# Kernel tuning notes

Measured on AMD Instinct MI355X. Metric: run time of the kernel, lower is better.

The kernel has to match this reference:

```python
import jax, jax.numpy as jnp
import numpy as np


def setup_inputs() -> dict:
    key = jax.random.key(0)
    x = jax.random.normal(key, (1024, 65536), dtype=jnp.float32)
    return {"input": x}


def reference(input) -> jnp.ndarray:
    B = input.shape[0]
    flat = input.reshape(B, -1)            # [B, N]
    N = flat.shape[1]
    idx = int(N * 0.8)                      # 80th-percentile position (ascending sort)
    cutoff = jnp.sort(flat, axis=-1)[:, idx]  # [B]
    cutoff = jax.lax.stop_gradient(cutoff)
    # broadcast cutoff back over all non-batch dims
    cutoff = cutoff.reshape((B,) + (1,) * (input.ndim - 1))
    return jax.nn.relu(input - cutoff)
```

## Files before the change

### kernel.cpp

```cpp
#include <hip/hip_runtime.h>


#define TPB1  1024
#define NB    4096
#define CAP   8192
#define TINY  64
#define BLO   0.72f
#define BHI   0.98f

#define TPB2  256
#define VPT   16

__device__ __forceinline__ unsigned f2ord(float f) {
    unsigned u = __float_as_uint(f);
    return (u & 0x80000000u) ? ~u : (u | 0x80000000u);
}
__device__ __forceinline__ float ord2f(unsigned u) {
    unsigned b = (u & 0x80000000u) ? (u ^ 0x80000000u) : ~u;
    return __uint_as_float(b);
}

__global__ __launch_bounds__(TPB1)
void cutoff_kernel(const float* __restrict__ in, float* __restrict__ cut,
                   int N, int k) {
    const int row  = blockIdx.x;
    const int tid  = threadIdx.x;
    const int lane = tid & 63;
    const int nv   = N >> 2;
    const float SCALE = (float)NB / (BHI - BLO);
    const float4* __restrict__ rowv = (const float4*)(in + (size_t)row * (size_t)N);

    __shared__ unsigned hist[NB];
    __shared__ unsigned cand[CAP];
    __shared__ unsigned part[TPB1];
    __shared__ unsigned tiny[TINY];
    __shared__ unsigned s_cnt, s_below, s_cum, s_tc;
    __shared__ int s_bin, s_fb;
    __shared__ float s_cut;

    for (int i = tid; i < NB; i += TPB1) hist[i] = 0u;
    if (tid == 0) { s_cnt = 0u; s_below = 0u; s_tc = 0u; s_fb = 0; }
    __syncthreads();

    unsigned below = 0;
    for (int i = tid; i < nv; i += TPB1) {
        float4 v = rowv[i];
        float vals[4] = {v.x, v.y, v.z, v.w};
        #pragma unroll
        for (int j = 0; j < 4; ++j) {
            float f = vals[j];
            below += (f < BLO) ? 1u : 0u;
            bool pred = (f >= BLO) && (f < BHI);
            unsigned long long m = __ballot(pred);
            if (m) {
                int leader = __ffsll((long long)m) - 1;
                unsigned base = 0;
                if (lane == leader) base = atomicAdd(&s_cnt, (unsigned)__popcll(m));
                base = __shfl(base, leader);
                if (pred) {
                    unsigned p = base + (unsigned)__popcll(m & ((1ull << lane) - 1ull));
                    if (p < CAP) cand[p] = __float_as_uint(f) | 0x80000000u;
                    int b = (int)((f - BLO) * SCALE);
                    b = b < 0 ? 0 : (b >= NB ? NB - 1 : b);
                    atomicAdd(&hist[b], 1u);
                }
            }
        }
    }
    #pragma unroll
    for (int o = 32; o > 0; o >>= 1) below += __shfl_down(below, o);
    if (lane == 0) atomicAdd(&s_below, below);
    __syncthreads();

    const unsigned M0 = s_cnt;
    const long long r2ll = (long long)k - (long long)s_below;

    if (M0 > CAP || r2ll < 0 || r2ll >= (long long)M0) {
        if (tid == 0) s_fb = 1;
    } else {
        const unsigned r2 = (unsigned)r2ll;
        const int base4 = tid * 4;
        unsigned s = hist[base4] + hist[base4 + 1] + hist[base4 + 2] + hist[base4 + 3];
        part[tid] = s;
        __syncthreads();
        for (int off = 1; off < TPB1; off <<= 1) {
            unsigned add = (tid >= off) ? part[tid - off] : 0u;
            __syncthreads();
            part[tid] += add;
            __syncthreads();
        }
        unsigned incl = part[tid], excl = incl - s;
        if (r2 >= excl && r2 < incl) {
            unsigned c = excl;
            #pragma unroll
            for (int j = 0; j < 4; ++j) {
                unsigned h = hist[base4 + j];
                if (r2 < c + h) { s_bin = base4 + j; s_cum = c; break; }
                c += h;
            }
        }
        __syncthreads();
        const int bin = s_bin;
        const unsigned r3 = r2 - s_cum;
        if (tid < 64) {
            for (unsigned i = (unsigned)lane; i < M0; i += 64u) {
                unsigned u = cand[i];
                float f = __uint_as_float(u ^ 0x80000000u);
                int b = (int)((f - BLO) * SCALE);
                b = b < 0 ? 0 : (b >= NB ? NB - 1 : b);
                bool pred = (b == bin);
                unsigned long long mm = __ballot(pred);
                if (mm) {
                    int leader = __ffsll((long long)mm) - 1;
                    unsigned tb = 0;
                    if (lane == leader) tb = atomicAdd(&s_tc, (unsigned)__popcll(mm));
                    tb = __shfl(tb, leader);
                    if (pred) {
                        unsigned p = tb + (unsigned)__popcll(mm & ((1ull << lane) - 1ull));
                        if (p < TINY) tiny[p] = u;
                    }
                }
            }
            unsigned c = s_tc;
            if (c > TINY) { if (lane == 0) s_fb = 1; }
            else {
                unsigned uj = (lane < (int)c) ? tiny[lane] : 0xFFFFFFFFu;
                unsigned less = 0, eq = 0;
                for (unsigned i2 = 0; i2 < c; ++i2) {
                    unsigned ui = tiny[i2];
                    less += (ui < uj) ? 1u : 0u;
                    eq   += (ui == uj) ? 1u : 0u;
                }
                bool cond = (lane < (int)c) && (less <= r3) && (r3 < less + eq);
                unsigned long long cm = __ballot(cond);
                if (cond && lane == __ffsll((long long)cm) - 1)
                    s_cut = __uint_as_float(uj ^ 0x80000000u);
            }
        }
    }
    __syncthreads();

    if (s_fb) {
        for (int i = tid; i < NB; i += TPB1) hist[i] = 0u;
        if (tid == 0) s_cnt = 0u;
        __syncthreads();
        for (int i = tid; i < nv; i += TPB1) {
            float4 v = rowv[i];
            float vals[4] = {v.x, v.y, v.z, v.w};
            #pragma unroll
            for (int j = 0; j < 4; ++j) atomicAdd(&hist[f2ord(vals[j]) >> 20], 1u);
        }
        __syncthreads();
        const int base4 = tid * 4;
        unsigned s = hist[base4] + hist[base4 + 1] + hist[base4 + 2] + hist[base4 + 3];
        part[tid] = s;
        __syncthreads();
        for (int off = 1; off < TPB1; off <<= 1) {
            unsigned add = (tid >= off) ? part[tid - off] : 0u;
            __syncthreads();
            part[tid] += add;
            __syncthreads();
        }
        const unsigned rk = (unsigned)k;
        unsigned incl = part[tid], excl = incl - s;
        if (rk >= excl && rk < incl) {
            unsigned c = excl;
            #pragma unroll
            for (int j = 0; j < 4; ++j) {
                unsigned h = hist[base4 + j];
                if (rk < c + h) { s_bin = base4 + j; s_cum = c; break; }
                c += h;
            }
        }
        __syncthreads();
        const unsigned bin = (unsigned)s_bin;
        for (int i = tid; i < nv; i += TPB1) {
            float4 v = rowv[i];
            float vals[4] = {v.x, v.y, v.z, v.w};
            #pragma unroll
            for (int j = 0; j < 4; ++j) {
                unsigned u = f2ord(vals[j]);
                bool pred = ((u >> 20) == bin);
                unsigned long long m = __ballot(pred);
                if (m) {
                    int leader = __ffsll((long long)m) - 1;
                    unsigned b2 = 0;
                    if (lane == leader) b2 = atomicAdd(&s_cnt, (unsigned)__popcll(m));
                    b2 = __shfl(b2, leader);
                    if (pred) {
                        unsigned p = b2 + (unsigned)__popcll(m & ((1ull << lane) - 1ull));
                        if (p < CAP) cand[p] = u;
                    }
                }
            }
        }
        __syncthreads();
        if (tid < 64) {
            unsigned M2 = s_cnt; if (M2 > CAP) M2 = CAP;
            unsigned prefix = bin;
            unsigned rr = (unsigned)k - s_cum;
            for (int bit = 19; bit >= 0; --bit) {
                unsigned want0 = prefix << 1;
                unsigned cnt = 0;
                for (unsigned i = (unsigned)lane; i < M2; i += 64u)
                    if ((cand[i] >> bit) == want0) cnt++;
                #pragma unroll
                for (int o = 32; o > 0; o >>= 1) cnt += __shfl_down(cnt, o);
                cnt = __shfl(cnt, 0);
                if (rr < cnt) prefix = want0;
                else { rr -= cnt; prefix = want0 | 1u; }
            }
            if (lane == 0) s_cut = ord2f(prefix);
        }
        __syncthreads();
    }

    if (tid == 0) cut[row] = s_cut;
}

__global__ __launch_bounds__(TPB2)
void relu_kernel(const float* __restrict__ in, const float* __restrict__ cut,
                 float* __restrict__ out, int N) {
    const int f4PerBlock = TPB2 * VPT;
    const int bpr = (N >> 2) / f4PerBlock;
    const int row = blockIdx.x / bpr;
    const float c = cut[row];
    const size_t base = (size_t)blockIdx.x * (size_t)f4PerBlock + threadIdx.x;
    const float4* __restrict__ iv = (const float4*)in;
    float4* __restrict__ ov = (float4*)out;
    #pragma unroll
    for (int j = 0; j < VPT; ++j) {
        size_t idx = base + (size_t)j * TPB2;
        float4 v = iv[idx];
        float4 o;
        o.x = fmaxf(v.x - c, 0.0f);
        o.y = fmaxf(v.y - c, 0.0f);
        o.z = fmaxf(v.z - c, 0.0f);
        o.w = fmaxf(v.w - c, 0.0f);
        ov[idx] = o;
    }
}

extern "C" void kernel_launch(void* const* d_in, const int* in_sizes, int n_in,
                              void* d_out, int out_size, void* d_ws, size_t ws_size,
                              hipStream_t stream) {
    const float* in = (const float*)d_in[0];
    float* out = (float*)d_out;
    float* cut = (float*)d_ws;
    const int N = 65536;
    const int B = in_sizes[0] / N;
    const int k = (int)(((long long)N * 4) / 5);

    cutoff_kernel<<<dim3(B), dim3(TPB1), 0, stream>>>(in, cut, N, k);

    const int totalF4 = (B * N) >> 2;
    const int blocks2 = totalF4 / (TPB2 * VPT);
    relu_kernel<<<dim3(blocks2), dim3(TPB2), 0, stream>>>(in, cut, out, N);
}
```

Baseline: 500.8 us.

## Shrink cutoff blocks, defer histogram to candidates, use wave-shuffle scan selection

```diff
diff --git a/kernel.cpp b/kernel.cpp
--- a/kernel.cpp
+++ b/kernel.cpp
@@ -1,9 +1,9 @@
 #include <hip/hip_runtime.h>
 
 
-#define TPB1  1024
-#define NB    4096
-#define CAP   8192
+#define TPB1  512
+#define NB    2048
+#define CAP   6144
 #define TINY  64
 #define BLO   0.72f
 #define BHI   0.98f
@@ -20,7 +20,39 @@
     return __uint_as_float(b);
 }
 
-__global__ __launch_bounds__(TPB1)
+__device__ __forceinline__ void hist_select(const unsigned* hist, unsigned r, int tid,
+                                            unsigned* wsum, unsigned* wbase,
+                                            int* s_bin, unsigned* s_cum) {
+    const int lane = tid & 63, wid = tid >> 6;
+    const int b0 = tid * (NB / TPB1);
+    unsigned h0 = hist[b0], h1 = hist[b0+1], h2 = hist[b0+2], h3 = hist[b0+3];
+    unsigned s = h0 + h1 + h2 + h3;
+    unsigned incl = s;
+    #pragma unroll
+    for (int off = 1; off < 64; off <<= 1) {
+        unsigned t = __shfl_up(incl, off);
+        if (lane >= off) incl += t;
+    }
+    if (lane == 63) wsum[wid] = incl;
+    __syncthreads();
+    if (tid == 0) {
+        unsigned c = 0;
+        #pragma unroll
+        for (int w = 0; w < TPB1/64; ++w) { wbase[w] = c; c += wsum[w]; }
+    }
+    __syncthreads();
+    unsigned excl = wbase[wid] + incl - s;
+    if (r >= excl && r < excl + s) {
+        unsigned c = excl;
+        if (r < c + h0)        { *s_bin = b0;     *s_cum = c; }
+        else { c += h0; if (r < c + h1) { *s_bin = b0 + 1; *s_cum = c; }
+        else { c += h1; if (r < c + h2) { *s_bin = b0 + 2; *s_cum = c; }
+        else { c += h2;                   *s_bin = b0 + 3; *s_cum = c; } } }
+    }
+    __syncthreads();
+}
+
+__global__ __launch_bounds__(TPB1, 8)
 void cutoff_kernel(const float* __restrict__ in, float* __restrict__ cut,
                    int N, int k) {
     const int row  = blockIdx.x;
@@ -32,8 +64,8 @@
 
     __shared__ unsigned hist[NB];
     __shared__ unsigned cand[CAP];
-    __shared__ unsigned part[TPB1];
     __shared__ unsigned tiny[TINY];
+    __shared__ unsigned wsum[TPB1/64], wbase[TPB1/64];
     __shared__ unsigned s_cnt, s_below, s_cum, s_tc;
     __shared__ int s_bin, s_fb;
     __shared__ float s_cut;
@@ -50,20 +82,9 @@
         for (int j = 0; j < 4; ++j) {
             float f = vals[j];
             below += (f < BLO) ? 1u : 0u;
-            bool pred = (f >= BLO) && (f < BHI);
-            unsigned long long m = __ballot(pred);
-            if (m) {
-                int leader = __ffsll((long long)m) - 1;
-                unsigned base = 0;
-                if (lane == leader) base = atomicAdd(&s_cnt, (unsigned)__popcll(m));
-                base = __shfl(base, leader);
-                if (pred) {
-                    unsigned p = base + (unsigned)__popcll(m & ((1ull << lane) - 1ull));
-                    if (p < CAP) cand[p] = __float_as_uint(f) | 0x80000000u;
-                    int b = (int)((f - BLO) * SCALE);
-                    b = b < 0 ? 0 : (b >= NB ? NB - 1 : b);
-                    atomicAdd(&hist[b], 1u);
-                }
+            if (f >= BLO && f < BHI) {
+                unsigned p = atomicAdd(&s_cnt, 1u);
+                if (p < CAP) cand[p] = __float_as_uint(f);
             }
         }
     }
@@ -74,144 +95,75 @@
 
     const unsigned M0 = s_cnt;
     const long long r2ll = (long long)k - (long long)s_below;
-
-    if (M0 > CAP || r2ll < 0 || r2ll >= (long long)M0) {
-        if (tid == 0) s_fb = 1;
-    } else {
+    const bool fast = (M0 <= CAP) && (r2ll >= 0) && (r2ll < (long long)M0);
+
+    if (fast) {
         const unsigned r2 = (unsigned)r2ll;
-        const int base4 = tid * 4;
-        unsigned s = hist[base4] + hist[base4 + 1] + hist[base4 + 2] + hist[base4 + 3];
-        part[tid] = s;
+        for (unsigned i = tid; i < M0; i += TPB1) {
+            float f = __uint_as_float(cand[i]);
+            int b = (int)((f - BLO) * SCALE);
+            b = b < 0 ? 0 : (b >= NB ? NB - 1 : b);
+            atomicAdd(&hist[b], 1u);
+        }
         __syncthreads();
-        for (int off = 1; off < TPB1; off <<= 1) {
-            unsigned add = (tid >= off) ? part[tid - off] : 0u;
-            __syncthreads();
-            part[tid] += add;
-            __syncthreads();
-        }
-        unsigned incl = part[tid], excl = incl - s;
-        if (r2 >= excl && r2 < incl) {
-            unsigned c = excl;
-            #pragma unroll
-            for (int j = 0; j < 4; ++j) {
-                unsigned h = hist[base4 + j];
-                if (r2 < c + h) { s_bin = base4 + j; s_cum = c; break; }
-                c += h;
-            }
-        }
-        __syncthreads();
+        hist_select(hist, r2, tid, wsum, wbase, &s_bin, &s_cum);
         const int bin = s_bin;
         const unsigned r3 = r2 - s_cum;
-        if (tid < 64) {
-            for (unsigned i = (unsigned)lane; i < M0; i += 64u) {
-                unsigned u = cand[i];
-                float f = __uint_as_float(u ^ 0x80000000u);
-                int b = (int)((f - BLO) * SCALE);
-                b = b < 0 ? 0 : (b >= NB ? NB - 1 : b);
-                bool pred = (b == bin);
-                unsigned long long mm = __ballot(pred);
-                if (mm) {
-                    int leader = __ffsll((long long)mm) - 1;
-                    unsigned tb = 0;
-                    if (lane == leader) tb = atomicAdd(&s_tc, (unsigned)__popcll(mm));
-                    tb = __shfl(tb, leader);
-                    if (pred) {
-                        unsigned p = tb + (unsigned)__popcll(mm & ((1ull << lane) - 1ull));
-                        if (p < TINY) tiny[p] = u;
-                    }
+        for (unsigned i = tid; i < M0; i += TPB1) {
+            unsigned u = cand[i];
+            float f = __uint_as_float(u);
+            int b = (int)((f - BLO) * SCALE);
+            b = b < 0 ? 0 : (b >= NB ? NB - 1 : b);
+            if (b == bin) { unsigned p = atomicAdd(&s_tc, 1u); if (p < TINY) tiny[p] = u; }
+        }
+        __syncthreads();
+        const unsigned c = s_tc;
+        if (c > TINY) { if (tid == 0) s_fb = 1; }
+        else if (tid < 64) {
+            unsigned uj = (lane < (int)c) ? tiny[lane] : 0xFFFFFFFFu;
+            unsigned less = 0, eq = 0;
+            for (unsigned i2 = 0; i2 < c; ++i2) {
+                unsigned ui = tiny[i2];
+                less += (ui < uj) ? 1u : 0u;
+                eq   += (ui == uj) ? 1u : 0u;
+            }
+            bool cond = (lane < (int)c) && (less <= r3) && (r3 < less + eq);
+            unsigned long long cm = __ballot(cond);
+            if (cond && lane == __ffsll((long long)cm) - 1)
+                s_cut = __uint_as_float(uj);
+        }
+    } else {
+        if (tid == 0) s_fb = 1;
+    }
+    __syncthreads();
+
+    if (s_fb) {
+        unsigned prefix = 0;
+        unsigned rr = (unsigned)k;
+        const int shifts[3] = {21, 10, 0};
+        const int bitsc[3]  = {11, 11, 10};
+        for (int pass = 0; pass < 3; ++pass) {
+            const int sh = shifts[pass];
+            const unsigned nb = 1u << bitsc[pass];
+            for (int i = tid; i < NB; i += TPB1) hist[i] = 0u;
+            __syncthreads();
+            for (int i = tid; i < nv; i += TPB1) {
+                float4 v = rowv[i];
+                float vals[4] = {v.x, v.y, v.z, v.w};
+                #pragma unroll
+                for (int j = 0; j < 4; ++j) {
+                    unsigned u = f2ord(vals[j]);
+                    if (pass == 0 || (u >> (sh + bitsc[pass])) == prefix)
+                        atomicAdd(&hist[(u >> sh) & (nb - 1u)], 1u);
                 }
             }
-            unsigned c = s_tc;
-            if (c > TINY) { if (lane == 0) s_fb = 1; }
-            else {
-                unsigned uj = (lane < (int)c) ? tiny[lane] : 0xFFFFFFFFu;
-                unsigned less = 0, eq = 0;
-                for (unsigned i2 = 0; i2 < c; ++i2) {
-                    unsigned ui = tiny[i2];
-                    less += (ui < uj) ? 1u : 0u;
-                    eq   += (ui == uj) ? 1u : 0u;
-                }
-                bool cond = (lane < (int)c) && (less <= r3) && (r3 < less + eq);
-                unsigned long long cm = __ballot(cond);
-                if (cond && lane == __ffsll((long long)cm) - 1)
-                    s_cut = __uint_as_float(uj ^ 0x80000000u);
-            }
-        }
-    }
-    __syncthreads();
-
-    if (s_fb) {
-        for (int i = tid; i < NB; i += TPB1) hist[i] = 0u;
-        if (tid == 0) s_cnt = 0u;
-        __syncthreads();
-        for (int i = tid; i < nv; i += TPB1) {
-            float4 v = rowv[i];
-            float vals[4] = {v.x, v.y, v.z, v.w};
-            #pragma unroll
-            for (int j = 0; j < 4; ++j) atomicAdd(&hist[f2ord(vals[j]) >> 20], 1u);
-        }
-        __syncthreads();
-        const int base4 = tid * 4;
-        unsigned s = hist[base4] + hist[base4 + 1] + hist[base4 + 2] + hist[base4 + 3];
-        part[tid] = s;
-        __syncthreads();
-        for (int off = 1; off < TPB1; off <<= 1) {
-            unsigned add = (tid >= off) ? part[tid - off] : 0u;
             __syncthreads();
-            part[tid] += add;
+            hist_select(hist, rr, tid, wsum, wbase, &s_bin, &s_cum);
+            prefix = (prefix << bitsc[pass]) | (unsigned)s_bin;
+            rr -= s_cum;
             __syncthreads();
         }
-        const unsigned rk = (unsigned)k;
-        unsigned incl = part[tid], excl = incl - s;
-        if (rk >= excl && rk < incl) {
-            unsigned c = excl;
-            #pragma unroll
-            for (int j = 0; j < 4; ++j) {
-                unsigned h = hist[base4 + j];
-                if (rk < c + h) { s_bin = base4 + j; s_cum = c; break; }
-                c += h;
-            }
-        }
-        __syncthreads();
-        const unsigned bin = (unsigned)s_bin;
-        for (int i = tid; i < nv; i += TPB1) {
-            float4 v = rowv[i];
-            float vals[4] = {v.x, v.y, v.z, v.w};
-            #pragma unroll
-            for (int j = 0; j < 4; ++j) {
-                unsigned u = f2ord(vals[j]);
-                bool pred = ((u >> 20) == bin);
-                unsigned long long m = __ballot(pred);
-                if (m) {
-                    int leader = __ffsll((long long)m) - 1;
-                    unsigned b2 = 0;
-                    if (lane == leader) b2 = atomicAdd(&s_cnt, (unsigned)__popcll(m));
-                    b2 = __shfl(b2, leader);
-                    if (pred) {
-                        unsigned p = b2 + (unsigned)__popcll(m & ((1ull << lane) - 1ull));
-                        if (p < CAP) cand[p] = u;
-                    }
-                }
-            }
-        }
-        __syncthreads();
-        if (tid < 64) {
-            unsigned M2 = s_cnt; if (M2 > CAP) M2 = CAP;
-            unsigned prefix = bin;
-            unsigned rr = (unsigned)k - s_cum;
-            for (int bit = 19; bit >= 0; --bit) {
-                unsigned want0 = prefix << 1;
-                unsigned cnt = 0;
-                for (unsigned i = (unsigned)lane; i < M2; i += 64u)
-                    if ((cand[i] >> bit) == want0) cnt++;
-                #pragma unroll
-                for (int o = 32; o > 0; o >>= 1) cnt += __shfl_down(cnt, o);
-                cnt = __shfl(cnt, 0);
-                if (rr < cnt) prefix = want0;
-                else { rr -= cnt; prefix = want0 | 1u; }
-            }
-            if (lane == 0) s_cut = ord2f(prefix);
-        }
+        if (tid == 0) s_cut = ord2f(prefix);
         __syncthreads();
     }
 
```

Measured after the change: 488.9 us. 1.02x faster.
